# Kernel tuning notes

Measured on AMD Instinct MI355X. Metric: run time of the kernel, lower is better.

The kernel has to match this reference:

```python
import jax, jax.numpy as jnp
import numpy as np

M = 4        # num_modalities
C = 128      # in_channels
NH = 4       # num_heads
HD = C // NH # head_dim = 32
OUT = 128    # out_channels
B, D, H, W = 1, 12, 12, 12
N = D * H * W
EPS = 1e-5
SCALE = float(np.sqrt(HD))


def setup_inputs() -> dict:
    key = jax.random.key(0)
    ks = jax.random.split(key, 12)
    inp = {}
    for i in range(M):
        inp[f"feat{i}"] = jax.random.normal(ks[i], (B, C, D, H, W), dtype=jnp.float32)
    s = 1.0 / np.sqrt(C)
    inp["Wq"] = jax.random.normal(ks[4], (M, C, C), dtype=jnp.float32) * s
    inp["Wk"] = jax.random.normal(ks[5], (M, C, C), dtype=jnp.float32) * s
    inp["Wv"] = jax.random.normal(ks[6], (M, C, C), dtype=jnp.float32) * s
    inp["Wout"] = jax.random.normal(ks[7], (OUT, C), dtype=jnp.float32) * s
    inp["bn_gamma"] = jnp.ones((OUT,), jnp.float32)
    inp["bn_beta"] = jnp.zeros((OUT,), jnp.float32)
    inp["bn_mean"] = jax.random.normal(ks[8], (OUT,), dtype=jnp.float32) * 0.1
    inp["bn_var"] = jax.random.uniform(ks[9], (OUT,), dtype=jnp.float32, minval=0.5, maxval=1.5)
    return inp


def _proj(Wm, feats):
    # per-modality 1x1 conv == matmul over channels: [M,C,C] x [M,B,C,N] -> [M,B,nh,N,hd]
    p = jnp.einsum('moc,mbcn->mbon', Wm, feats)
    return p.reshape(M, B, NH, HD, N).transpose(0, 1, 2, 4, 3)


def reference(feat0, feat1, feat2, feat3, Wq, Wk, Wv, Wout,
              bn_gamma, bn_beta, bn_mean, bn_var):
    feats = jnp.stack([feat0, feat1, feat2, feat3]).reshape(M, B, C, N)
    Q = _proj(Wq, feats)   # [M,B,nh,N,hd]
    K = _proj(Wk, feats)
    V = _proj(Wv, feats)
    # concat K/V over modalities along token axis -> [B,nh,M*N,hd]
    Kall = K.transpose(1, 2, 0, 3, 4).reshape(B, NH, M * N, HD)
    Vall = V.transpose(1, 2, 0, 3, 4).reshape(B, NH, M * N, HD)
    fused = jnp.zeros((B, NH, N, HD), jnp.float32)
    for i in range(M):  # small fixed loop over modalities
        attn = jnp.einsum('bhqd,bhkd->bhqk', Q[i], Kall) / SCALE  # [B,nh,N,M*N]
        attn = jax.nn.softmax(attn, axis=-1)  # dropout is identity at eval
        fused = fused + jnp.einsum('bhqk,bhkd->bhqd', attn, Vall)
    fused = fused.transpose(0, 1, 3, 2).reshape(B, C, N)
    # out_proj: 1x1 Conv3d -> BN (eval, running stats) -> ReLU
    y = jnp.einsum('oc,bcn->bon', Wout, fused)
    inv = bn_gamma / jnp.sqrt(bn_var + EPS)
    y = y * inv[None, :, None] + (bn_beta - bn_mean * inv)[None, :, None]
    return jax.nn.relu(y).reshape(B, OUT, D, H, W)
```

## Files before the change

### kernel.cpp

```cpp
#include <hip/hip_runtime.h>

#define MODS 4
#define CH   128
#define NHD  4
#define HDIM 32
#define NTOK 1728
#define NKEY (MODS*NTOK)
#define NT   27
#define QSC (0.17677669529663687f * 1.4426950408889634f)

#ifndef __has_builtin
#define __has_builtin(x) 0
#endif
#if __has_builtin(__builtin_amdgcn_exp2f)
#define EXP2(x) __builtin_amdgcn_exp2f(x)
#else
#define EXP2(x) __expf(0.69314718055994531f * (x))
#endif

typedef __bf16 bf16x8 __attribute__((ext_vector_type(8)));
typedef float  f32x16 __attribute__((ext_vector_type(16)));

__device__ inline bf16x8 ldb8(const unsigned short* p) {
    return *reinterpret_cast<const bf16x8*>(p);
}
__device__ inline unsigned short bfc(float x) {
    return __builtin_bit_cast(unsigned short, (__bf16)x);
}
__device__ inline unsigned int pkbf(float a, float b) {
    return (unsigned int)bfc(a) | ((unsigned int)bfc(b) << 16);
}
__device__ inline void glds16(const unsigned short* g, unsigned short* l) {
    __builtin_amdgcn_global_load_lds(
        (const __attribute__((address_space(1))) unsigned int*)(g),
        (__attribute__((address_space(3))) unsigned int*)(l), 16, 0, 0);
}

__global__ __launch_bounds__(256) void prepw_kernel(
    const float* __restrict__ Wq, const float* __restrict__ Wk,
    const float* __restrict__ Wv, const float* __restrict__ Wout,
    unsigned short* __restrict__ Wb, unsigned short* __restrict__ WbO)
{
    const int gid = blockIdx.x * 256 + threadIdx.x;
    const size_t base = (size_t)gid * 16;
    const float* src; unsigned short* dst; float sc = 1.0f;
    if (base < 65536)       { src = Wq + base;            dst = Wb + base;  sc = QSC; }
    else if (base < 131072) { src = Wk + (base - 65536);  dst = Wb + base; }
    else if (base < 196608) { src = Wv + (base - 131072); dst = Wb + base; }
    else                    { src = Wout + (base - 196608); dst = WbO + (base - 196608); }
    #pragma unroll
    for (int g = 0; g < 4; ++g) {
        float4 v = *reinterpret_cast<const float4*>(src + g * 4);
        ushort4 pk;
        pk.x = bfc(v.x * sc); pk.y = bfc(v.y * sc);
        pk.z = bfc(v.z * sc); pk.w = bfc(v.w * sc);
        *reinterpret_cast<ushort4*>(dst + g * 4) = pk;
    }
}

__global__ __launch_bounds__(256) void proj_kernel(
    const float* __restrict__ f0, const float* __restrict__ f1,
    const float* __restrict__ f2, const float* __restrict__ f3,
    const unsigned short* __restrict__ Wb,
    unsigned short* __restrict__ Qb, unsigned short* __restrict__ Kb,
    unsigned short* __restrict__ V2)
{
    __shared__ __align__(16) unsigned short fT[32][136];
    __shared__ __align__(16) float accf[128 * 33];

    const int tid = threadIdx.x;
    const int lane = tid & 63;
    const int w    = tid >> 6;
    const int l31  = lane & 31;
    const int hi   = lane >> 5;

    const int bid = blockIdx.x;
    const int tm  = bid / 54;
    const int nb  = (bid % 54) * 32;
    const int t   = tm >> 2, m = tm & 3;

    const float* fsrc = (m == 0) ? f0 : (m == 1) ? f1 : (m == 2) ? f2 : f3;

    {
        const int n = tid & 31, cg = tid >> 5;
        float v[16];
        #pragma unroll
        for (int k = 0; k < 16; ++k)
            v[k] = fsrc[(size_t)(cg * 16 + k) * NTOK + nb + n];
        unsigned int* dst = reinterpret_cast<unsigned int*>(&fT[n][cg * 16]);
        #pragma unroll
        for (int j = 0; j < 8; ++j) dst[j] = pkbf(v[2 * j], v[2 * j + 1]);
    }
    __syncthreads();

    const unsigned short* Wrow = Wb + ((size_t)tm * CH + w * 32 + l31) * CH + hi * 8;
    f32x16 acc;
    #pragma unroll
    for (int r = 0; r < 16; ++r) acc[r] = 0.f;
    #pragma unroll
    for (int cc = 0; cc < 8; ++cc) {
        bf16x8 a = ldb8(Wrow + cc * 16);
        bf16x8 b = ldb8(&fT[l31][cc * 16 + hi * 8]);
        acc = __builtin_amdgcn_mfma_f32_32x32x16_bf16(a, b, acc, 0, 0, 0);
    }
    #pragma unroll
    for (int r = 0; r < 16; ++r) {
        const int orow = w * 32 + (r & 3) + 8 * (r >> 2) + 4 * hi;
        accf[orow * 33 + l31] = acc[r];
    }
    __syncthreads();

    if (t < 2) {
        unsigned short* dstb = (t == 0) ? Qb : Kb;
        const int nl = tid >> 3, dp = (tid & 7) * 4;
        #pragma unroll
        for (int h = 0; h < 4; ++h) {
            ushort4 pk;
            pk.x = bfc(accf[(h * 32 + dp + 0) * 33 + nl]);
            pk.y = bfc(accf[(h * 32 + dp + 1) * 33 + nl]);
            pk.z = bfc(accf[(h * 32 + dp + 2) * 33 + nl]);
            pk.w = bfc(accf[(h * 32 + dp + 3) * 33 + nl]);
            *reinterpret_cast<ushort4*>(
                dstb + (((size_t)(m * NHD + h)) * NTOK + nb + nl) * HDIM + dp) = pk;
        }
    } else {
        const int row = tid >> 1, half = tid & 1;
        const int nw = half * 16;
        unsigned short* dst = V2 + (size_t)row * NKEY + (size_t)m * NTOK + nb + nw;
        const float* src = &accf[row * 33 + nw];
        ushort4 p0, p1, p2, p3;
        p0.x = bfc(src[0]);  p0.y = bfc(src[1]);  p0.z = bfc(src[2]);  p0.w = bfc(src[3]);
        p1.x = bfc(src[8]);  p1.y = bfc(src[9]);  p1.z = bfc(src[10]); p1.w = bfc(src[11]);
        p2.x = bfc(src[4]);  p2.y = bfc(src[5]);  p2.z = bfc(src[6]);  p2.w = bfc(src[7]);
        p3.x = bfc(src[12]); p3.y = bfc(src[13]); p3.z = bfc(src[14]); p3.w = bfc(src[15]);
        *reinterpret_cast<ushort4*>(dst + 0)  = p0;
        *reinterpret_cast<ushort4*>(dst + 4)  = p1;
        *reinterpret_cast<ushort4*>(dst + 8)  = p2;
        *reinterpret_cast<ushort4*>(dst + 12) = p3;
    }
}

__global__ __launch_bounds__(256, 6) void attn_kernel(
    const unsigned short* __restrict__ Qb, const unsigned short* __restrict__ Kb,
    const unsigned short* __restrict__ V2,
    float* __restrict__ accT, float* __restrict__ sR)
{
    __shared__ __align__(16) unsigned short smAll[2][2][2][1024];

    const int tid  = threadIdx.x;
    const int lane = tid & 63;
    const int w    = tid >> 6;
    const int qslot = w & 1;
    const int ks    = w >> 1;
    const int l31  = lane & 31;
    const int hi   = lane >> 5;

    const int bid  = blockIdx.x;
    const int slot = bid & 7;
    const int h    = slot >> 1;
    const int ko   = slot & 1;
    const int rest = bid >> 3;
    const int qb   = rest % 108;
    const int kseg = rest / 108;
    const int qtile = qb * 2 + qslot;
    const int qg0  = qtile * 32;
    const int im   = qg0 / NTOK;
    const int n0   = qg0 % NTOK;
    const int km   = ko * 2 + ks;
    const int p    = kseg * 2 + ko;

    const unsigned short* qp = Qb + (((size_t)(im * NHD + h)) * NTOK + n0 + l31) * HDIM + hi * 8;
    const bf16x8 qf0 = ldb8(qp);
    const bf16x8 qf1 = ldb8(qp + 16);

    const int rk0 = qslot * 16 + (lane >> 2);
    const int ck0 = (lane & 3) ^ ((rk0 >> 1) & 3);
    const unsigned short* gk0 = Kb
        + (((size_t)(km * NHD + h)) * NTOK + kseg * 864 + rk0) * HDIM + ck0 * 8;
    const int dv0 = qslot * 16 + (lane >> 2);
    const int cv0 = (lane & 3) ^ (dv0 & 3);
    const unsigned short* gv0 = V2
        + ((size_t)(h * HDIM + dv0)) * NKEY + km * NTOK + kseg * 864 + cv0 * 8;

    const int fK = (l31 >> 1) & 3, fV = l31 & 3;
    const int kA0 = l31 * 32 + ((hi ^ fK) << 3);
    const int kB0 = l31 * 32 + (((2 + hi) ^ fK) << 3);
    const int vo0 = l31 * 32 + ((hi ^ fV) << 3);
    const int vo1 = l31 * 32 + (((2 + hi) ^ fV) << 3);

    f32x16 z;
    #pragma unroll
    for (int r = 0; r < 16; ++r) z[r] = 0.f;
    f32x16 o_acc = z, s_acc = z;
    bf16x8 onesv;
    #pragma unroll
    for (int j = 0; j < 8; ++j) onesv[j] = (__bf16)1.0f;

    #define STAGE(bb) do {                                      \
        glds16(gk0, &smAll[bb][ks][0][0] + qslot * 512);        \
        glds16(gv0, &smAll[bb][ks][1][0] + qslot * 512);        \
        gk0 += 1024; gv0 += 32;                                 \
    } while (0)

    STAGE(0);
    __syncthreads();

    int buf = 0;
    for (int t = 0; t < NT; ++t) {
        if (t + 1 < NT) STAGE(buf ^ 1);
        const unsigned short* Kl = &smAll[buf][ks][0][0];
        const unsigned short* Vl = &smAll[buf][ks][1][0];

        bf16x8 k0 = ldb8(Kl + kA0);
        bf16x8 k1 = ldb8(Kl + kB0);
        f32x16 c = __builtin_amdgcn_mfma_f32_32x32x16_bf16(k0, qf0, z, 0, 0, 0);
        c = __builtin_amdgcn_mfma_f32_32x32x16_bf16(k1, qf1, c, 0, 0, 0);

        float e[16];
        #pragma unroll
        for (int r = 0; r < 16; ++r) e[r] = EXP2(c[r]);
        bf16x8 pa0, pa1;
        #pragma unroll
        for (int j = 0; j < 8; ++j) { pa0[j] = (__bf16)e[j]; pa1[j] = (__bf16)e[8 + j]; }

        bf16x8 v0 = ldb8(Vl + vo0);
        bf16x8 v1 = ldb8(Vl + vo1);

        o_acc = __builtin_amdgcn_mfma_f32_32x32x16_bf16(pa0, v0, o_acc, 0, 0, 0);
        o_acc = __builtin_amdgcn_mfma_f32_32x32x16_bf16(pa1, v1, o_acc, 0, 0, 0);
        s_acc = __builtin_amdgcn_mfma_f32_32x32x16_bf16(pa0, onesv, s_acc, 0, 0, 0);
        s_acc = __builtin_amdgcn_mfma_f32_32x32x16_bf16(pa1, onesv, s_acc, 0, 0, 0);

        __syncthreads();
        buf ^= 1;
    }
    #undef STAGE

    float* accfL = (float*)&smAll[0][0][0][0];
    if (ks == 1) {
        #pragma unroll
        for (int r = 0; r < 16; ++r) {
            const int qrow = (r & 3) + 8 * (r >> 2) + 4 * hi;
            accfL[(qslot * 32 + qrow) * 33 + l31] = o_acc[r];
            if (l31 == 0) accfL[(qslot * 32 + qrow) * 33 + 32] = s_acc[r];
        }
    }
    __syncthreads();
    if (ks == 0) {
        #pragma unroll
        for (int r = 0; r < 16; ++r) {
            const int qrow = (r & 3) + 8 * (r >> 2) + 4 * hi;
            accfL[(qslot * 32 + qrow) * 33 + l31] += o_acc[r];
            if (l31 == 0) accfL[(qslot * 32 + qrow) * 33 + 32] += s_acc[r];
        }
    }
    __syncthreads();
    {
        const int q  = tid & 63;
        const int dq = tid >> 6;
        #pragma unroll
        for (int j = 0; j < 8; ++j) {
            const int d = dq * 8 + j;
            accT[((size_t)((p * 4 + h) * HDIM + d)) * NKEY + (size_t)qb * 64 + q]
                = accfL[q * 33 + d];
        }
        if (tid < 64)
            sR[((size_t)(p * 4 + h)) * NKEY + (size_t)qb * 64 + tid] = accfL[tid * 33 + 32];
    }
}

__global__ __launch_bounds__(256) void normout_kernel(
    const float* __restrict__ accT, const float* __restrict__ sR,
    const unsigned short* __restrict__ WbO,
    const float* __restrict__ gamma, const float* __restrict__ beta,
    const float* __restrict__ mean,  const float* __restrict__ var,
    float* __restrict__ out)
{
    __shared__ __align__(16) unsigned short fT2[32][136];
    __shared__ float rsL[4][4][32];

    const int tid = threadIdx.x;
    const int nb  = blockIdx.x * 32;

    #pragma unroll
    for (int e2 = 0; e2 < 2; ++e2) {
        const int e = tid * 2 + e2;
        const int h = e >> 7, imq = (e >> 5) & 3, n = e & 31;
        float s = 0.f;
        #pragma unroll
        for (int pp = 0; pp < 4; ++pp)
            s += sR[(size_t)(pp * 4 + h) * NKEY + (size_t)imq * NTOK + nb + n];
        rsL[h][imq][n] = 1.0f / s;
    }
    __syncthreads();

    {
        const int n4 = (tid & 7) * 4;
        const int c0 = (tid >> 3) * 4;
        const int h  = c0 >> 5;
        float acc4[4][4] = {};
        #pragma unroll
        for (int imq = 0; imq < 4; ++imq) {
            const size_t q = (size_t)imq * NTOK + nb + n4;
            float a[4][4] = {};
            #pragma unroll
            for (int pp = 0; pp < 4; ++pp) {
                #pragma unroll
                for (int cc = 0; cc < 4; ++cc) {
                    const int d = (c0 + cc) & 31;
                    float4 x = *reinterpret_cast<const float4*>(
                        accT + ((size_t)((pp * 4 + h) * HDIM + d)) * NKEY + q);
                    a[cc][0] += x.x; a[cc][1] += x.y; a[cc][2] += x.z; a[cc][3] += x.w;
                }
            }
            #pragma unroll
            for (int cc = 0; cc < 4; ++cc)
                #pragma unroll
                for (int nn = 0; nn < 4; ++nn)
                    acc4[cc][nn] = fmaf(a[cc][nn], rsL[h][imq][n4 + nn], acc4[cc][nn]);
        }
        #pragma unroll
        for (int nn = 0; nn < 4; ++nn) {
            ushort4 pk;
            pk.x = bfc(acc4[0][nn]); pk.y = bfc(acc4[1][nn]);
            pk.z = bfc(acc4[2][nn]); pk.w = bfc(acc4[3][nn]);
            *reinterpret_cast<ushort4*>(&fT2[n4 + nn][c0]) = pk;
        }
    }
    __syncthreads();

    {
        const int lane = tid & 63;
        const int w    = tid >> 6;
        const int l31  = lane & 31;
        const int hi   = lane >> 5;
        const unsigned short* Arow = WbO + (size_t)(w * 32 + l31) * CH + hi * 8;
        f32x16 acc;
        #pragma unroll
        for (int r = 0; r < 16; ++r) acc[r] = 0.f;
        #pragma unroll
        for (int cc = 0; cc < 8; ++cc) {
            bf16x8 a = ldb8(Arow + cc * 16);
            bf16x8 b = ldb8(&fT2[l31][cc * 16 + hi * 8]);
            acc = __builtin_amdgcn_mfma_f32_32x32x16_bf16(a, b, acc, 0, 0, 0);
        }
        #pragma unroll
        for (int r = 0; r < 16; ++r) {
            const int orow = w * 32 + (r & 3) + 8 * (r >> 2) + 4 * hi;
            const float inv = gamma[orow] * rsqrtf(var[orow] + 1e-5f);
            const float sh  = fmaf(-mean[orow], inv, beta[orow]);
            out[(size_t)orow * NTOK + nb + l31] = fmaxf(fmaf(acc[r], inv, sh), 0.f);
        }
    }
}

extern "C" void kernel_launch(void* const* d_in, const int* in_sizes, int n_in,
                              void* d_out, int out_size, void* d_ws, size_t ws_size,
                              hipStream_t stream)
{
    const float* f0    = (const float*)d_in[0];
    const float* f1    = (const float*)d_in[1];
    const float* f2    = (const float*)d_in[2];
    const float* f3    = (const float*)d_in[3];
    const float* Wq    = (const float*)d_in[4];
    const float* Wk    = (const float*)d_in[5];
    const float* Wv    = (const float*)d_in[6];
    const float* Wout  = (const float*)d_in[7];
    const float* gamma = (const float*)d_in[8];
    const float* beta  = (const float*)d_in[9];
    const float* mean  = (const float*)d_in[10];
    const float* var   = (const float*)d_in[11];
    float* out = (float*)d_out;

    const size_t QKV = (size_t)MODS * NHD * NTOK * HDIM;
    unsigned short* Qb  = (unsigned short*)d_ws;
    unsigned short* Kb  = Qb + QKV;
    unsigned short* V2  = Kb + QKV;
    unsigned short* Wb  = V2 + QKV;
    unsigned short* WbO = Wb + 196608;
    float* accT = (float*)(WbO + 16384);
    float* sR   = accT + (size_t)512 * NKEY;

    prepw_kernel<<<52, 256, 0, stream>>>(Wq, Wk, Wv, Wout, Wb, WbO);
    proj_kernel<<<648, 256, 0, stream>>>(f0, f1, f2, f3, Wb, Qb, Kb, V2);
    attn_kernel<<<1728, 256, 0, stream>>>(Qb, Kb, V2, accT, sR);
    normout_kernel<<<54, 256, 0, stream>>>(
        accT, sR, WbO, gamma, beta, mean, var, out);
}
```

Measured before the change: 70.81 us.

## Drop weight prep kernel, double query tiles per attention warp, widen normout

```diff
diff --git a/kernel.cpp b/kernel.cpp
--- a/kernel.cpp
+++ b/kernel.cpp
@@ -20,6 +20,7 @@
 
 typedef __bf16 bf16x8 __attribute__((ext_vector_type(8)));
 typedef float  f32x16 __attribute__((ext_vector_type(16)));
+typedef unsigned int u32x4 __attribute__((ext_vector_type(4)));
 
 __device__ inline bf16x8 ldb8(const unsigned short* p) {
     return *reinterpret_cast<const bf16x8*>(p);
@@ -29,6 +30,13 @@
 }
 __device__ inline unsigned int pkbf(float a, float b) {
     return (unsigned int)bfc(a) | ((unsigned int)bfc(b) << 16);
+}
+__device__ inline bf16x8 cvt8(const float* p, float sc) {
+    float4 x = *reinterpret_cast<const float4*>(p);
+    float4 y = *reinterpret_cast<const float4*>(p + 4);
+    u32x4 u = {pkbf(x.x * sc, x.y * sc), pkbf(x.z * sc, x.w * sc),
+               pkbf(y.x * sc, y.y * sc), pkbf(y.z * sc, y.w * sc)};
+    return __builtin_bit_cast(bf16x8, u);
 }
 __device__ inline void glds16(const unsigned short* g, unsigned short* l) {
     __builtin_amdgcn_global_load_lds(
@@ -36,32 +44,11 @@
         (__attribute__((address_space(3))) unsigned int*)(l), 16, 0, 0);
 }
 
-__global__ __launch_bounds__(256) void prepw_kernel(
-    const float* __restrict__ Wq, const float* __restrict__ Wk,
-    const float* __restrict__ Wv, const float* __restrict__ Wout,
-    unsigned short* __restrict__ Wb, unsigned short* __restrict__ WbO)
-{
-    const int gid = blockIdx.x * 256 + threadIdx.x;
-    const size_t base = (size_t)gid * 16;
-    const float* src; unsigned short* dst; float sc = 1.0f;
-    if (base < 65536)       { src = Wq + base;            dst = Wb + base;  sc = QSC; }
-    else if (base < 131072) { src = Wk + (base - 65536);  dst = Wb + base; }
-    else if (base < 196608) { src = Wv + (base - 131072); dst = Wb + base; }
-    else                    { src = Wout + (base - 196608); dst = WbO + (base - 196608); }
-    #pragma unroll
-    for (int g = 0; g < 4; ++g) {
-        float4 v = *reinterpret_cast<const float4*>(src + g * 4);
-        ushort4 pk;
-        pk.x = bfc(v.x * sc); pk.y = bfc(v.y * sc);
-        pk.z = bfc(v.z * sc); pk.w = bfc(v.w * sc);
-        *reinterpret_cast<ushort4*>(dst + g * 4) = pk;
-    }
-}
-
 __global__ __launch_bounds__(256) void proj_kernel(
     const float* __restrict__ f0, const float* __restrict__ f1,
     const float* __restrict__ f2, const float* __restrict__ f3,
-    const unsigned short* __restrict__ Wb,
+    const float* __restrict__ Wq, const float* __restrict__ Wk,
+    const float* __restrict__ Wv,
     unsigned short* __restrict__ Qb, unsigned short* __restrict__ Kb,
     unsigned short* __restrict__ V2)
 {
@@ -80,6 +67,8 @@
     const int t   = tm >> 2, m = tm & 3;
 
     const float* fsrc = (m == 0) ? f0 : (m == 1) ? f1 : (m == 2) ? f2 : f3;
+    const float* Wsrc = ((t == 0) ? Wq : (t == 1) ? Wk : Wv) + (size_t)m * CH * CH;
+    const float  wsc  = (t == 0) ? QSC : 1.0f;
 
     {
         const int n = tid & 31, cg = tid >> 5;
@@ -93,13 +82,13 @@
     }
     __syncthreads();
 
-    const unsigned short* Wrow = Wb + ((size_t)tm * CH + w * 32 + l31) * CH + hi * 8;
+    const float* Wrow = Wsrc + (size_t)(w * 32 + l31) * CH + hi * 8;
     f32x16 acc;
     #pragma unroll
     for (int r = 0; r < 16; ++r) acc[r] = 0.f;
     #pragma unroll
     for (int cc = 0; cc < 8; ++cc) {
-        bf16x8 a = ldb8(Wrow + cc * 16);
+        bf16x8 a = cvt8(Wrow + cc * 16, wsc);
         bf16x8 b = ldb8(&fT[l31][cc * 16 + hi * 8]);
         acc = __builtin_amdgcn_mfma_f32_32x32x16_bf16(a, b, acc, 0, 0, 0);
     }
@@ -140,17 +129,18 @@
     }
 }
 
-__global__ __launch_bounds__(256, 6) void attn_kernel(
+__global__ __launch_bounds__(256, 3) void attn_kernel(
     const unsigned short* __restrict__ Qb, const unsigned short* __restrict__ Kb,
     const unsigned short* __restrict__ V2,
     float* __restrict__ accT, float* __restrict__ sR)
 {
-    __shared__ __align__(16) unsigned short smAll[2][2][2][1024];
+    __shared__ __align__(16) unsigned char smraw[16896];
+    unsigned short* smb = (unsigned short*)smraw;
 
     const int tid  = threadIdx.x;
     const int lane = tid & 63;
     const int w    = tid >> 6;
-    const int qslot = w & 1;
+    const int qpair = w & 1;
     const int ks    = w >> 1;
     const int l31  = lane & 31;
     const int hi   = lane >> 5;
@@ -160,24 +150,26 @@
     const int h    = slot >> 1;
     const int ko   = slot & 1;
     const int rest = bid >> 3;
-    const int qb   = rest % 108;
-    const int kseg = rest / 108;
-    const int qtile = qb * 2 + qslot;
-    const int qg0  = qtile * 32;
-    const int im   = qg0 / NTOK;
-    const int n0   = qg0 % NTOK;
+    const int qgrp = rest % 54;
+    const int kseg = rest / 54;
     const int km   = ko * 2 + ks;
     const int p    = kseg * 2 + ko;
 
-    const unsigned short* qp = Qb + (((size_t)(im * NHD + h)) * NTOK + n0 + l31) * HDIM + hi * 8;
-    const bf16x8 qf0 = ldb8(qp);
-    const bf16x8 qf1 = ldb8(qp + 16);
-
-    const int rk0 = qslot * 16 + (lane >> 2);
+    const int qtile0 = qgrp * 4 + qpair * 2;
+    const int qg0 = qtile0 * 32, qg1 = qg0 + 32;
+    const int im0 = qg0 / NTOK, n00 = qg0 % NTOK;
+    const int im1 = qg1 / NTOK, n01 = qg1 % NTOK;
+
+    const unsigned short* qpA = Qb + (((size_t)(im0 * NHD + h)) * NTOK + n00 + l31) * HDIM + hi * 8;
+    const unsigned short* qpB = Qb + (((size_t)(im1 * NHD + h)) * NTOK + n01 + l31) * HDIM + hi * 8;
+    const bf16x8 qfA0 = ldb8(qpA), qfA1 = ldb8(qpA + 16);
+    const bf16x8 qfB0 = ldb8(qpB), qfB1 = ldb8(qpB + 16);
+
+    const int rk0 = qpair * 16 + (lane >> 2);
     const int ck0 = (lane & 3) ^ ((rk0 >> 1) & 3);
     const unsigned short* gk0 = Kb
         + (((size_t)(km * NHD + h)) * NTOK + kseg * 864 + rk0) * HDIM + ck0 * 8;
-    const int dv0 = qslot * 16 + (lane >> 2);
+    const int dv0 = qpair * 16 + (lane >> 2);
     const int cv0 = (lane & 3) ^ (dv0 & 3);
     const unsigned short* gv0 = V2
         + ((size_t)(h * HDIM + dv0)) * NKEY + km * NTOK + kseg * 864 + cv0 * 8;
@@ -191,15 +183,15 @@
     f32x16 z;
     #pragma unroll
     for (int r = 0; r < 16; ++r) z[r] = 0.f;
-    f32x16 o_acc = z, s_acc = z;
+    f32x16 o_accA = z, o_accB = z, s_accA = z, s_accB = z;
     bf16x8 onesv;
     #pragma unroll
     for (int j = 0; j < 8; ++j) onesv[j] = (__bf16)1.0f;
 
-    #define STAGE(bb) do {                                      \
-        glds16(gk0, &smAll[bb][ks][0][0] + qslot * 512);        \
-        glds16(gv0, &smAll[bb][ks][1][0] + qslot * 512);        \
-        gk0 += 1024; gv0 += 32;                                 \
+    #define STAGE(bb) do {                                              \
+        glds16(gk0, smb + (((bb) * 2 + ks) * 2) * 1024 + qpair * 512);  \
+        glds16(gv0, smb + (((bb) * 2 + ks) * 2 + 1) * 1024 + qpair * 512); \
+        gk0 += 1024; gv0 += 32;                                         \
     } while (0)
 
     STAGE(0);
@@ -208,41 +200,57 @@
     int buf = 0;
     for (int t = 0; t < NT; ++t) {
         if (t + 1 < NT) STAGE(buf ^ 1);
-        const unsigned short* Kl = &smAll[buf][ks][0][0];
-        const unsigned short* Vl = &smAll[buf][ks][1][0];
+        const unsigned short* Kl = smb + ((buf * 2 + ks) * 2) * 1024;
+        const unsigned short* Vl = Kl + 1024;
 
         bf16x8 k0 = ldb8(Kl + kA0);
         bf16x8 k1 = ldb8(Kl + kB0);
-        f32x16 c = __builtin_amdgcn_mfma_f32_32x32x16_bf16(k0, qf0, z, 0, 0, 0);
-        c = __builtin_amdgcn_mfma_f32_32x32x16_bf16(k1, qf1, c, 0, 0, 0);
-
-        float e[16];
-        #pragma unroll
-        for (int r = 0; r < 16; ++r) e[r] = EXP2(c[r]);
-        bf16x8 pa0, pa1;
-        #pragma unroll
-        for (int j = 0; j < 8; ++j) { pa0[j] = (__bf16)e[j]; pa1[j] = (__bf16)e[8 + j]; }
+        f32x16 cA = __builtin_amdgcn_mfma_f32_32x32x16_bf16(k0, qfA0, z, 0, 0, 0);
+        cA = __builtin_amdgcn_mfma_f32_32x32x16_bf16(k1, qfA1, cA, 0, 0, 0);
+        float eA[16];
+        #pragma unroll
+        for (int r = 0; r < 16; ++r) eA[r] = EXP2(cA[r]);
+        bf16x8 paA0, paA1;
+        #pragma unroll
+        for (int j = 0; j < 8; ++j) { paA0[j] = (__bf16)eA[j]; paA1[j] = (__bf16)eA[8 + j]; }
+        f32x16 cB = __builtin_amdgcn_mfma_f32_32x32x16_bf16(k0, qfB0, z, 0, 0, 0);
+        cB = __builtin_amdgcn_mfma_f32_32x32x16_bf16(k1, qfB1, cB, 0, 0, 0);
+        float eB[16];
+        #pragma unroll
+        for (int r = 0; r < 16; ++r) eB[r] = EXP2(cB[r]);
+        bf16x8 paB0, paB1;
+        #pragma unroll
+        for (int j = 0; j < 8; ++j) { paB0[j] = (__bf16)eB[j]; paB1[j] = (__bf16)eB[8 + j]; }
 
         bf16x8 v0 = ldb8(Vl + vo0);
         bf16x8 v1 = ldb8(Vl + vo1);
 
-        o_acc = __builtin_amdgcn_mfma_f32_32x32x16_bf16(pa0, v0, o_acc, 0, 0, 0);
-        o_acc = __builtin_amdgcn_mfma_f32_32x32x16_bf16(pa1, v1, o_acc, 0, 0, 0);
-        s_acc = __builtin_amdgcn_mfma_f32_32x32x16_bf16(pa0, onesv, s_acc, 0, 0, 0);
-        s_acc = __builtin_amdgcn_mfma_f32_32x32x16_bf16(pa1, onesv, s_acc, 0, 0, 0);
+        o_accA = __builtin_amdgcn_mfma_f32_32x32x16_bf16(paA0, v0, o_accA, 0, 0, 0);
+        o_accA = __builtin_amdgcn_mfma_f32_32x32x16_bf16(paA1, v1, o_accA, 0, 0, 0);
+        o_accB = __builtin_amdgcn_mfma_f32_32x32x16_bf16(paB0, v0, o_accB, 0, 0, 0);
+        o_accB = __builtin_amdgcn_mfma_f32_32x32x16_bf16(paB1, v1, o_accB, 0, 0, 0);
+        s_accA = __builtin_amdgcn_mfma_f32_32x32x16_bf16(paA0, onesv, s_accA, 0, 0, 0);
+        s_accA = __builtin_amdgcn_mfma_f32_32x32x16_bf16(paA1, onesv, s_accA, 0, 0, 0);
+        s_accB = __builtin_amdgcn_mfma_f32_32x32x16_bf16(paB0, onesv, s_accB, 0, 0, 0);
+        s_accB = __builtin_amdgcn_mfma_f32_32x32x16_bf16(paB1, onesv, s_accB, 0, 0, 0);
 
         __syncthreads();
         buf ^= 1;
     }
     #undef STAGE
 
-    float* accfL = (float*)&smAll[0][0][0][0];
+    float* accfL = (float*)smraw;
+    const int tiA = qpair * 2, tiB = tiA + 1;
     if (ks == 1) {
         #pragma unroll
         for (int r = 0; r < 16; ++r) {
             const int qrow = (r & 3) + 8 * (r >> 2) + 4 * hi;
-            accfL[(qslot * 32 + qrow) * 33 + l31] = o_acc[r];
-            if (l31 == 0) accfL[(qslot * 32 + qrow) * 33 + 32] = s_acc[r];
+            accfL[(tiA * 32 + qrow) * 33 + l31] = o_accA[r];
+            accfL[(tiB * 32 + qrow) * 33 + l31] = o_accB[r];
+            if (l31 == 0) {
+                accfL[(tiA * 32 + qrow) * 33 + 32] = s_accA[r];
+                accfL[(tiB * 32 + qrow) * 33 + 32] = s_accB[r];
+            }
         }
     }
     __syncthreads();
@@ -250,28 +258,32 @@
         #pragma unroll
         for (int r = 0; r < 16; ++r) {
             const int qrow = (r & 3) + 8 * (r >> 2) + 4 * hi;
-            accfL[(qslot * 32 + qrow) * 33 + l31] += o_acc[r];
-            if (l31 == 0) accfL[(qslot * 32 + qrow) * 33 + 32] += s_acc[r];
+            accfL[(tiA * 32 + qrow) * 33 + l31] += o_accA[r];
+            accfL[(tiB * 32 + qrow) * 33 + l31] += o_accB[r];
+            if (l31 == 0) {
+                accfL[(tiA * 32 + qrow) * 33 + 32] += s_accA[r];
+                accfL[(tiB * 32 + qrow) * 33 + 32] += s_accB[r];
+            }
         }
     }
     __syncthreads();
     {
-        const int q  = tid & 63;
-        const int dq = tid >> 6;
-        #pragma unroll
-        for (int j = 0; j < 8; ++j) {
-            const int d = dq * 8 + j;
-            accT[((size_t)((p * 4 + h) * HDIM + d)) * NKEY + (size_t)qb * 64 + q]
-                = accfL[q * 33 + d];
-        }
-        if (tid < 64)
-            sR[((size_t)(p * 4 + h)) * NKEY + (size_t)qb * 64 + tid] = accfL[tid * 33 + 32];
-    }
-}
-
-__global__ __launch_bounds__(256) void normout_kernel(
+        const int q2  = tid & 127;
+        const int dq2 = tid >> 7;
+        #pragma unroll
+        for (int j = 0; j < 16; ++j) {
+            const int d = dq2 * 16 + j;
+            accT[((size_t)((p * 4 + h) * HDIM + d)) * NKEY + (size_t)qgrp * 128 + q2]
+                = accfL[q2 * 33 + d];
+        }
+        if (tid < 128)
+            sR[((size_t)(p * 4 + h)) * NKEY + (size_t)qgrp * 128 + tid] = accfL[tid * 33 + 32];
+    }
+}
+
+__global__ __launch_bounds__(512) void normout_kernel(
     const float* __restrict__ accT, const float* __restrict__ sR,
-    const unsigned short* __restrict__ WbO,
+    const float* __restrict__ Wout,
     const float* __restrict__ gamma, const float* __restrict__ beta,
     const float* __restrict__ mean,  const float* __restrict__ var,
     float* __restrict__ out)
@@ -282,10 +294,8 @@
     const int tid = threadIdx.x;
     const int nb  = blockIdx.x * 32;
 
-    #pragma unroll
-    for (int e2 = 0; e2 < 2; ++e2) {
-        const int e = tid * 2 + e2;
-        const int h = e >> 7, imq = (e >> 5) & 3, n = e & 31;
+    {
+        const int h = tid >> 7, imq = (tid >> 5) & 3, n = tid & 31;
         float s = 0.f;
         #pragma unroll
         for (int pp = 0; pp < 4; ++pp)
@@ -296,17 +306,17 @@
 
     {
         const int n4 = (tid & 7) * 4;
-        const int c0 = (tid >> 3) * 4;
+        const int c0 = (tid >> 3) * 2;
         const int h  = c0 >> 5;
-        float acc4[4][4] = {};
+        float acc4[2][4] = {};
         #pragma unroll
         for (int imq = 0; imq < 4; ++imq) {
             const size_t q = (size_t)imq * NTOK + nb + n4;
-            float a[4][4] = {};
+            float a[2][4] = {};
             #pragma unroll
             for (int pp = 0; pp < 4; ++pp) {
                 #pragma unroll
-                for (int cc = 0; cc < 4; ++cc) {
+                for (int cc = 0; cc < 2; ++cc) {
                     const int d = (c0 + cc) & 31;
                     float4 x = *reinterpret_cast<const float4*>(
                         accT + ((size_t)((pp * 4 + h) * HDIM + d)) * NKEY + q);
@@ -314,33 +324,32 @@
                 }
             }
             #pragma unroll
-            for (int cc = 0; cc < 4; ++cc)
+            for (int cc = 0; cc < 2; ++cc)
                 #pragma unroll
                 for (int nn = 0; nn < 4; ++nn)
                     acc4[cc][nn] = fmaf(a[cc][nn], rsL[h][imq][n4 + nn], acc4[cc][nn]);
         }
         #pragma unroll
         for (int nn = 0; nn < 4; ++nn) {
-            ushort4 pk;
+            ushort2 pk;
             pk.x = bfc(acc4[0][nn]); pk.y = bfc(acc4[1][nn]);
-            pk.z = bfc(acc4[2][nn]); pk.w = bfc(acc4[3][nn]);
-            *reinterpret_cast<ushort4*>(&fT2[n4 + nn][c0]) = pk;
-        }
-    }
-    __syncthreads();
-
-    {
+            *reinterpret_cast<ushort2*>(&fT2[n4 + nn][c0]) = pk;
+        }
+    }
+    __syncthreads();
+
+    if (tid < 256) {
         const int lane = tid & 63;
         const int w    = tid >> 6;
         const int l31  = lane & 31;
         const int hi   = lane >> 5;
-        const unsigned short* Arow = WbO + (size_t)(w * 32 + l31) * CH + hi * 8;
+        const float* Arow = Wout + (size_t)(w * 32 + l31) * CH + hi * 8;
         f32x16 acc;
         #pragma unroll
         for (int r = 0; r < 16; ++r) acc[r] = 0.f;
         #pragma unroll
         for (int cc = 0; cc < 8; ++cc) {
-            bf16x8 a = ldb8(Arow + cc * 16);
+            bf16x8 a = cvt8(Arow + cc * 16, 1.0f);
             bf16x8 b = ldb8(&fT2[l31][cc * 16 + hi * 8]);
             acc = __builtin_amdgcn_mfma_f32_32x32x16_bf16(a, b, acc, 0, 0, 0);
         }
@@ -376,14 +385,11 @@
     unsigned short* Qb  = (unsigned short*)d_ws;
     unsigned short* Kb  = Qb + QKV;
     unsigned short* V2  = Kb + QKV;
-    unsigned short* Wb  = V2 + QKV;
-    unsigned short* WbO = Wb + 196608;
-    float* accT = (float*)(WbO + 16384);
+    float* accT = (float*)(V2 + QKV);
     float* sR   = accT + (size_t)512 * NKEY;
 
-    prepw_kernel<<<52, 256, 0, stream>>>(Wq, Wk, Wv, Wout, Wb, WbO);
-    proj_kernel<<<648, 256, 0, stream>>>(f0, f1, f2, f3, Wb, Qb, Kb, V2);
-    attn_kernel<<<1728, 256, 0, stream>>>(Qb, Kb, V2, accT, sR);
-    normout_kernel<<<54, 256, 0, stream>>>(
-        accT, sR, WbO, gamma, beta, mean, var, out);
-}
+    proj_kernel<<<648, 256, 0, stream>>>(f0, f1, f2, f3, Wq, Wk, Wv, Qb, Kb, V2);
+    attn_kernel<<<864, 256, 0, stream>>>(Qb, Kb, V2, accT, sR);
+    normout_kernel<<<54, 512, 0, stream>>>(
+        accT, sR, Wout, gamma, beta, mean, var, out);
+}
```

New measurement: 71.46 us. Within noise of the previous version (+0.9%).
